# Performance work log

Hardware: AMD Instinct MI355X
Metric: run time of the kernel (lower is better)

The kernel has to match this reference:

```python
import jax, jax.numpy as jnp
import numpy as np

B, S, D = 2048, 8, 1280
K = 1                 # n_components_remove
HIGH_T = 0.6          # PC1_HIGH_ACTIVITY_THRESHOLD
STORM_T = 0.8         # solar_storm_threshold


def setup_inputs() -> dict:
    key = jax.random.key(0)
    k1, k2 = jax.random.split(key, 2)
    features = jax.random.normal(k1, (B, S, D), dtype=jnp.float32)
    kp_index = jax.random.uniform(k2, (B,), dtype=jnp.float32) * 9.0
    cmr_gate = jnp.ones((1,), dtype=jnp.float32)  # nn.Parameter(torch.ones(1))
    return {"features": features, "kp_index": kp_index, "cmr_gate": cmr_gate}


def reference(features, kp_index, cmr_gate):
    # Per-sample standardization over the feature axis (numpy std, ddof=0)
    mu = features.mean(axis=2, keepdims=True)            # (B, S, 1)
    sigma = features.std(axis=2, keepdims=True) + 1e-8   # (B, S, 1)
    fn = (features - mu) / sigma                         # (B, S, D)

    # Batched thin SVD of the (S, D) normalized feature matrix
    U, sv, Vt = jnp.linalg.svd(fn, full_matrices=False)  # (B,S,S), (B,S), (B,S,D)
    var = sv * sv
    pc1_ratio = var[:, 0] / (var.sum(axis=-1) + 1e-8)    # (B,)

    # solar_flag: 0 normal, 1 high activity, 2 storm
    solar_flag = (pc1_ratio >= HIGH_T).astype(jnp.int32) + (pc1_ratio >= STORM_T).astype(jnp.int32)

    # Rank-K reconstruction of the common-mode (solar) component
    low = jnp.einsum('bsk,bk,bkd->bsd', U[:, :, :K], sv[:, :K], Vt[:, :K, :])
    clean = (fn - low) * sigma + mu                      # de-normalized cleaned features

    # Kp-gating: amplify CMR when Kp >= 5
    kp_gate = 1.0 + 0.5 * (kp_index >= 5.0).astype(features.dtype)[:, None, None]
    clean = features + kp_gate * (clean - features)

    # Learnable gate
    gate = jax.nn.sigmoid(cmr_gate)[0]
    features_clean = features + gate * (clean - features)
    return features_clean, pc1_ratio, solar_flag
```

## Files before the change

kernel.cpp:

```cpp
#include <hip/hip_runtime.h>
#include <math.h>


#define SV 8
#define DV 1280
#define D4 320
#define BSTRIDE (SV*DV)
#define GSZ 136
#define SPLIT 4
#define CITER (40/SPLIT)

typedef __attribute__((ext_vector_type(8))) short bf16x8;
typedef __attribute__((ext_vector_type(4))) float f32x4;

union BF8 { bf16x8 v; short s[8]; unsigned u[4]; };

__global__ __launch_bounds__(256, 2)
void cmr_fused(const float* __restrict__ feat,
               const float* __restrict__ kp,
               const float* __restrict__ cmr_gate,
               float* __restrict__ out, int Bn)
{
    __shared__ float lg[SPLIT][2][GSZ];
    __shared__ float lc[2][17];

    const int tid  = threadIdx.x;
    const int lane = tid & 63;
    const int h    = tid >> 6;
    const int pair = blockIdx.x;

    {
        const int m    = lane & 15;
        const int quad = lane >> 4;
        const int bt   = m >> 3;
        const int row  = m & 7;

        const float* __restrict__ fb =
            feat + ((size_t)(pair * 2 + bt)) * BSTRIDE + (size_t)row * DV;

        BF8 ones;
#pragma unroll
        for (int j = 0; j < 4; ++j) ones.u[j] = 0x3F803F80u;

        f32x4 accHH = {0.f, 0.f, 0.f, 0.f};
        f32x4 accHL = {0.f, 0.f, 0.f, 0.f};
        f32x4 accS  = {0.f, 0.f, 0.f, 0.f};

#pragma unroll
        for (int c = 0; c < CITER; ++c) {
            const int k0 = (h * CITER + c) * 32 + quad * 8;
            const float4 x0 = *(const float4*)(fb + k0);
            const float4 x1 = *(const float4*)(fb + k0 + 4);
            float x[8] = {x0.x, x0.y, x0.z, x0.w, x1.x, x1.y, x1.z, x1.w};
            BF8 hi, lo;
#pragma unroll
            for (int j = 0; j < 4; ++j) {
                unsigned hp, lp;
                asm("v_cvt_pk_bf16_f32 %0, %1, %2"
                    : "=v"(hp) : "v"(x[2*j]), "v"(x[2*j+1]));
                const float h0 = __uint_as_float(hp << 16);
                const float h1 = __uint_as_float(hp & 0xFFFF0000u);
                const float l0 = x[2*j]     - h0;
                const float l1 = x[2*j + 1] - h1;
                asm("v_cvt_pk_bf16_f32 %0, %1, %2"
                    : "=v"(lp) : "v"(l0), "v"(l1));
                hi.u[j] = hp;
                lo.u[j] = lp;
            }
            accHH = __builtin_amdgcn_mfma_f32_16x16x32_bf16(hi.v, hi.v,   accHH, 0, 0, 0);
            accHL = __builtin_amdgcn_mfma_f32_16x16x32_bf16(hi.v, lo.v,   accHL, 0, 0, 0);
            accS  = __builtin_amdgcn_mfma_f32_16x16x32_bf16(hi.v, ones.v, accS,  0, 0, 0);
            accS  = __builtin_amdgcn_mfma_f32_16x16x32_bf16(lo.v, ones.v, accS,  0, 0, 0);
        }

        const int colb = (lane & 15) >> 3;
        const int col  = lane & 7;
#pragma unroll
        for (int r = 0; r < 4; ++r) {
            const int rowg = quad * 4 + r;
            if ((rowg >> 3) == colb) {
                lg[h][colb][(rowg & 7) * 8 + col]      = accHH[r];
                lg[h][colb][64 + (rowg & 7) * 8 + col] = accHL[r];
            }
        }
        if ((lane & 15) == 0) {
#pragma unroll
            for (int r = 0; r < 4; ++r) {
                const int rowg = quad * 4 + r;
                lg[h][rowg >> 3][128 + (rowg & 7)] = accS[r];
            }
        }
    }
    __syncthreads();

    if (h == 0 && lane < 2) {
        const int b2 = lane;
        const int b  = pair * 2 + b2;

        float G[8][8], S[8], mu[8], sig[8], rsig[8];
#pragma unroll
        for (int i = 0; i < 8; ++i) {
#pragma unroll
            for (int j = 0; j < 8; ++j) G[i][j] = 0.f;
            S[i] = 0.f;
        }
#pragma unroll
        for (int hh = 0; hh < SPLIT; ++hh) {
            const float* __restrict__ gh = &lg[hh][b2][0];
#pragma unroll
            for (int i = 0; i < 8; ++i) {
#pragma unroll
                for (int j = 0; j < 8; ++j)
                    G[i][j] += gh[i * 8 + j] + gh[64 + i * 8 + j] + gh[64 + j * 8 + i];
                S[i] += gh[128 + i];
            }
        }
        const float invD = 1.f / (float)DV;
#pragma unroll
        for (int i = 0; i < 8; ++i) {
            mu[i] = S[i] * invD;
            const float var = fmaxf(G[i][i] * invD - mu[i] * mu[i], 0.f);
            sig[i]  = sqrtf(var) + 1e-8f;
            rsig[i] = 1.f / sig[i];
        }
#pragma unroll
        for (int i = 0; i < 8; ++i)
#pragma unroll
            for (int j = 0; j < 8; ++j)
                G[i][j] = (G[i][j] - (float)DV * mu[i] * mu[j]) * rsig[i] * rsig[j];

        float tr = 0.f;
#pragma unroll
        for (int i = 0; i < 8; ++i) tr += G[i][i];

        float A[8][8];
        {
            const float rt = 1.f / fmaxf(tr, 1e-30f);
#pragma unroll
            for (int i = 0; i < 8; ++i)
#pragma unroll
                for (int j = 0; j < 8; ++j) A[i][j] = G[i][j] * rt;
        }
#pragma unroll
        for (int t = 0; t < 12; ++t) {
            float Bm[8][8];
            float trB = 0.f;
#pragma unroll
            for (int i = 0; i < 8; ++i)
#pragma unroll
                for (int j = i; j < 8; ++j) {
                    float acc = 0.f;
#pragma unroll
                    for (int k = 0; k < 8; ++k)
                        acc = fmaf(A[i][k], A[j][k], acc);
                    Bm[i][j] = acc;
                    if (i == j) trB += acc;
                }
            const float rt = 1.f / fmaxf(trB, 1e-30f);
#pragma unroll
            for (int i = 0; i < 8; ++i)
#pragma unroll
                for (int j = i; j < 8; ++j) {
                    const float v = Bm[i][j] * rt;
                    A[i][j] = v; A[j][i] = v;
                }
        }
        int bj = 0; float best = A[0][0];
#pragma unroll
        for (int k = 1; k < 8; ++k)
            if (A[k][k] > best) { best = A[k][k]; bj = k; }
        float u[8];
#pragma unroll
        for (int i = 0; i < 8; ++i) {
            float v = A[i][0];
#pragma unroll
            for (int k = 1; k < 8; ++k) v = (bj == k) ? A[i][k] : v;
            u[i] = v;
        }
        {
            float nn = 0.f;
#pragma unroll
            for (int i = 0; i < 8; ++i) nn = fmaf(u[i], u[i], nn);
            const float r = rsqrtf(fmaxf(nn, 1e-30f));
#pragma unroll
            for (int i = 0; i < 8; ++i) u[i] *= r;
        }
#pragma unroll
        for (int it = 0; it < 2; ++it) {
            float y[8]; float ny = 0.f;
#pragma unroll
            for (int i = 0; i < 8; ++i) {
                float acc = 0.f;
#pragma unroll
                for (int k = 0; k < 8; ++k) acc = fmaf(G[i][k], u[k], acc);
                y[i] = acc; ny = fmaf(acc, acc, ny);
            }
            const float r = rsqrtf(fmaxf(ny, 1e-30f));
#pragma unroll
            for (int i = 0; i < 8; ++i) u[i] = y[i] * r;
        }
        float lam = 0.f;
#pragma unroll
        for (int i = 0; i < 8; ++i) {
            float acc = 0.f;
#pragma unroll
            for (int k = 0; k < 8; ++k) acc = fmaf(G[i][k], u[k], acc);
            lam = fmaf(u[i], acc, lam);
        }
        const float pc1 = lam / (tr + 1e-8f);

        const float gate = 1.f / (1.f + expf(-cmr_gate[0]));
        const float kpg  = (kp[b] >= 5.0f) ? 1.5f : 1.0f;
        const float Gt   = gate * kpg;

        float bc = 0.f;
#pragma unroll
        for (int i = 0; i < 8; ++i) bc = fmaf(u[i] * rsig[i], mu[i], bc);

#pragma unroll
        for (int i = 0; i < 8; ++i) {
            lc[b2][i]     = u[i] * rsig[i];
            lc[b2][8 + i] = Gt * sig[i] * u[i];
        }
        lc[b2][16] = bc;
        out[(size_t)Bn * BSTRIDE + b] = pc1;
        out[(size_t)Bn * BSTRIDE + Bn + b] =
            (pc1 >= 0.6f ? 1.f : 0.f) + (pc1 >= 0.8f ? 1.f : 0.f);
    }
    __syncthreads();

    for (int u = tid; u < 2 * D4; u += 256) {
        const int b2  = (u >= D4) ? 1 : 0;
        const int col = u - b2 * D4;

        float a[8], c[8];
#pragma unroll
        for (int s = 0; s < 8; ++s) { a[s] = lc[b2][s]; c[s] = lc[b2][8 + s]; }
        const float bc = lc[b2][16];

        const float4* __restrict__ f4 =
            (const float4*)(feat + (size_t)(pair * 2 + b2) * BSTRIDE);
        float4* __restrict__ o4 =
            (float4*)(out + (size_t)(pair * 2 + b2) * BSTRIDE);

        float4 f[8];
#pragma unroll
        for (int s = 0; s < 8; ++s) f[s] = f4[s * D4 + col];

        float4 p = make_float4(-bc, -bc, -bc, -bc);
#pragma unroll
        for (int s = 0; s < 8; ++s) {
            p.x = fmaf(a[s], f[s].x, p.x);
            p.y = fmaf(a[s], f[s].y, p.y);
            p.z = fmaf(a[s], f[s].z, p.z);
            p.w = fmaf(a[s], f[s].w, p.w);
        }
#pragma unroll
        for (int s = 0; s < 8; ++s) {
            float4 o;
            o.x = fmaf(-c[s], p.x, f[s].x);
            o.y = fmaf(-c[s], p.y, f[s].y);
            o.z = fmaf(-c[s], p.z, f[s].z);
            o.w = fmaf(-c[s], p.w, f[s].w);
            o4[s * D4 + col] = o;
        }
    }
}

extern "C" void kernel_launch(void* const* d_in, const int* in_sizes, int n_in,
                              void* d_out, int out_size, void* d_ws, size_t ws_size,
                              hipStream_t stream) {
    const float* feat = (const float*)d_in[0];
    const float* kp   = (const float*)d_in[1];
    const float* gate = (const float*)d_in[2];
    float* out = (float*)d_out;
    const int Bn = in_sizes[0] / BSTRIDE;
    (void)d_ws; (void)ws_size;

    cmr_fused<<<Bn / 2, 256, 0, stream>>>(feat, kp, gate, out, Bn);
}
```

Baseline: 178.0 us.

## Rewrite as one-wavefront-per-sample kernel holding features in registers

Replaces the 256-thread, two-sample block with a single 64-lane wavefront per batch sample. The wavefront loads the whole 8x1280 slice into registers once, computes the Gram matrix in fp32 FMAs with shuffle reductions in place of split-bf16 MFMAs, and every lane runs the redundant 8x8 eigen solve. The output pass then reuses the register-resident data instead of reloading features from global memory, and LDS and block barriers are gone. In exchange it needs about 160 VGPRs for the data plus the symmetric matrices, which caps occupancy. The serial eigen-solve latency is also no longer hidden behind other waves in the block.

Measured after the change: 171.6 us. 3.6% less time.

```diff
diff --git a/kernel.cpp b/kernel.cpp
--- a/kernel.cpp
+++ b/kernel.cpp
@@ -6,263 +6,201 @@
 #define DV 1280
 #define D4 320
 #define BSTRIDE (SV*DV)
-#define GSZ 136
-#define SPLIT 4
-#define CITER (40/SPLIT)
-
-typedef __attribute__((ext_vector_type(8))) short bf16x8;
-typedef __attribute__((ext_vector_type(4))) float f32x4;
-
-union BF8 { bf16x8 v; short s[8]; unsigned u[4]; };
-
-__global__ __launch_bounds__(256, 2)
-void cmr_fused(const float* __restrict__ feat,
-               const float* __restrict__ kp,
-               const float* __restrict__ cmr_gate,
-               float* __restrict__ out, int Bn)
+
+__device__ __forceinline__ float wsum(float v) {
+    v += __shfl_xor(v, 32);
+    v += __shfl_xor(v, 16);
+    v += __shfl_xor(v, 8);
+    v += __shfl_xor(v, 4);
+    v += __shfl_xor(v, 2);
+    v += __shfl_xor(v, 1);
+    return v;
+}
+
+#define GU(i,k) ((i) <= (k) ? G[i][k] : G[k][i])
+#define AU(i,k) ((i) <= (k) ? A[i][k] : A[k][i])
+
+__global__ __launch_bounds__(64, 1)
+void cmr_wave(const float* __restrict__ feat,
+              const float* __restrict__ kp,
+              const float* __restrict__ cmr_gate,
+              float* __restrict__ out, int Bn)
 {
-    __shared__ float lg[SPLIT][2][GSZ];
-    __shared__ float lc[2][17];
-
-    const int tid  = threadIdx.x;
-    const int lane = tid & 63;
-    const int h    = tid >> 6;
-    const int pair = blockIdx.x;
-
+    const int lane = threadIdx.x;
+    const int b    = blockIdx.x;
+
+    const float4* __restrict__ f4 =
+        (const float4*)(feat + (size_t)b * BSTRIDE);
+
+    float4 f[8][5];
+#pragma unroll
+    for (int s = 0; s < 8; ++s)
+#pragma unroll
+        for (int c = 0; c < 5; ++c)
+            f[s][c] = f4[s * D4 + c * 64 + lane];
+
+    float G[8][8];
+    float S[8];
+#pragma unroll
+    for (int i = 0; i < 8; ++i) {
+        S[i] = 0.f;
+#pragma unroll
+        for (int j = i; j < 8; ++j) G[i][j] = 0.f;
+    }
+#pragma unroll
+    for (int c = 0; c < 5; ++c) {
+#pragma unroll
+        for (int i = 0; i < 8; ++i) {
+            const float4 a = f[i][c];
+            S[i] += (a.x + a.y) + (a.z + a.w);
+#pragma unroll
+            for (int j = i; j < 8; ++j) {
+                const float4 q = f[j][c];
+                G[i][j] = fmaf(a.x, q.x,
+                          fmaf(a.y, q.y,
+                          fmaf(a.z, q.z,
+                          fmaf(a.w, q.w, G[i][j]))));
+            }
+        }
+    }
+#pragma unroll
+    for (int i = 0; i < 8; ++i) {
+        S[i] = wsum(S[i]);
+#pragma unroll
+        for (int j = i; j < 8; ++j) G[i][j] = wsum(G[i][j]);
+    }
+
+    float mu[8], sig[8], rsig[8];
+    const float invD = 1.f / (float)DV;
+#pragma unroll
+    for (int i = 0; i < 8; ++i) {
+        mu[i] = S[i] * invD;
+        const float var = fmaxf(G[i][i] * invD - mu[i] * mu[i], 0.f);
+        sig[i]  = sqrtf(var) + 1e-8f;
+        rsig[i] = 1.f / sig[i];
+    }
+#pragma unroll
+    for (int i = 0; i < 8; ++i)
+#pragma unroll
+        for (int j = i; j < 8; ++j)
+            G[i][j] = (G[i][j] - (float)DV * mu[i] * mu[j]) * rsig[i] * rsig[j];
+
+    float tr = 0.f;
+#pragma unroll
+    for (int i = 0; i < 8; ++i) tr += G[i][i];
+
+    float A[8][8];
     {
-        const int m    = lane & 15;
-        const int quad = lane >> 4;
-        const int bt   = m >> 3;
-        const int row  = m & 7;
-
-        const float* __restrict__ fb =
-            feat + ((size_t)(pair * 2 + bt)) * BSTRIDE + (size_t)row * DV;
-
-        BF8 ones;
-#pragma unroll
-        for (int j = 0; j < 4; ++j) ones.u[j] = 0x3F803F80u;
-
-        f32x4 accHH = {0.f, 0.f, 0.f, 0.f};
-        f32x4 accHL = {0.f, 0.f, 0.f, 0.f};
-        f32x4 accS  = {0.f, 0.f, 0.f, 0.f};
-
-#pragma unroll
-        for (int c = 0; c < CITER; ++c) {
-            const int k0 = (h * CITER + c) * 32 + quad * 8;
-            const float4 x0 = *(const float4*)(fb + k0);
-            const float4 x1 = *(const float4*)(fb + k0 + 4);
-            float x[8] = {x0.x, x0.y, x0.z, x0.w, x1.x, x1.y, x1.z, x1.w};
-            BF8 hi, lo;
-#pragma unroll
-            for (int j = 0; j < 4; ++j) {
-                unsigned hp, lp;
-                asm("v_cvt_pk_bf16_f32 %0, %1, %2"
-                    : "=v"(hp) : "v"(x[2*j]), "v"(x[2*j+1]));
-                const float h0 = __uint_as_float(hp << 16);
-                const float h1 = __uint_as_float(hp & 0xFFFF0000u);
-                const float l0 = x[2*j]     - h0;
-                const float l1 = x[2*j + 1] - h1;
-                asm("v_cvt_pk_bf16_f32 %0, %1, %2"
-                    : "=v"(lp) : "v"(l0), "v"(l1));
-                hi.u[j] = hp;
-                lo.u[j] = lp;
+        const float rt = 1.f / fmaxf(tr, 1e-30f);
+#pragma unroll
+        for (int i = 0; i < 8; ++i)
+#pragma unroll
+            for (int j = i; j < 8; ++j) A[i][j] = G[i][j] * rt;
+    }
+#pragma unroll
+    for (int t = 0; t < 12; ++t) {
+        float Bm[8][8];
+        float trB = 0.f;
+#pragma unroll
+        for (int i = 0; i < 8; ++i)
+#pragma unroll
+            for (int j = i; j < 8; ++j) {
+                float acc = 0.f;
+#pragma unroll
+                for (int k = 0; k < 8; ++k)
+                    acc = fmaf(AU(i, k), AU(j, k), acc);
+                Bm[i][j] = acc;
+                if (i == j) trB += acc;
             }
-            accHH = __builtin_amdgcn_mfma_f32_16x16x32_bf16(hi.v, hi.v,   accHH, 0, 0, 0);
-            accHL = __builtin_amdgcn_mfma_f32_16x16x32_bf16(hi.v, lo.v,   accHL, 0, 0, 0);
-            accS  = __builtin_amdgcn_mfma_f32_16x16x32_bf16(hi.v, ones.v, accS,  0, 0, 0);
-            accS  = __builtin_amdgcn_mfma_f32_16x16x32_bf16(lo.v, ones.v, accS,  0, 0, 0);
-        }
-
-        const int colb = (lane & 15) >> 3;
-        const int col  = lane & 7;
-#pragma unroll
-        for (int r = 0; r < 4; ++r) {
-            const int rowg = quad * 4 + r;
-            if ((rowg >> 3) == colb) {
-                lg[h][colb][(rowg & 7) * 8 + col]      = accHH[r];
-                lg[h][colb][64 + (rowg & 7) * 8 + col] = accHL[r];
-            }
-        }
-        if ((lane & 15) == 0) {
-#pragma unroll
-            for (int r = 0; r < 4; ++r) {
-                const int rowg = quad * 4 + r;
-                lg[h][rowg >> 3][128 + (rowg & 7)] = accS[r];
-            }
-        }
-    }
-    __syncthreads();
-
-    if (h == 0 && lane < 2) {
-        const int b2 = lane;
-        const int b  = pair * 2 + b2;
-
-        float G[8][8], S[8], mu[8], sig[8], rsig[8];
-#pragma unroll
-        for (int i = 0; i < 8; ++i) {
-#pragma unroll
-            for (int j = 0; j < 8; ++j) G[i][j] = 0.f;
-            S[i] = 0.f;
-        }
-#pragma unroll
-        for (int hh = 0; hh < SPLIT; ++hh) {
-            const float* __restrict__ gh = &lg[hh][b2][0];
-#pragma unroll
-            for (int i = 0; i < 8; ++i) {
-#pragma unroll
-                for (int j = 0; j < 8; ++j)
-                    G[i][j] += gh[i * 8 + j] + gh[64 + i * 8 + j] + gh[64 + j * 8 + i];
-                S[i] += gh[128 + i];
-            }
-        }
-        const float invD = 1.f / (float)DV;
-#pragma unroll
-        for (int i = 0; i < 8; ++i) {
-            mu[i] = S[i] * invD;
-            const float var = fmaxf(G[i][i] * invD - mu[i] * mu[i], 0.f);
-            sig[i]  = sqrtf(var) + 1e-8f;
-            rsig[i] = 1.f / sig[i];
-        }
+        const float rt = 1.f / fmaxf(trB, 1e-30f);
 #pragma unroll
         for (int i = 0; i < 8; ++i)
 #pragma unroll
-            for (int j = 0; j < 8; ++j)
-                G[i][j] = (G[i][j] - (float)DV * mu[i] * mu[j]) * rsig[i] * rsig[j];
-
-        float tr = 0.f;
-#pragma unroll
-        for (int i = 0; i < 8; ++i) tr += G[i][i];
-
-        float A[8][8];
-        {
-            const float rt = 1.f / fmaxf(tr, 1e-30f);
-#pragma unroll
-            for (int i = 0; i < 8; ++i)
-#pragma unroll
-                for (int j = 0; j < 8; ++j) A[i][j] = G[i][j] * rt;
-        }
-#pragma unroll
-        for (int t = 0; t < 12; ++t) {
-            float Bm[8][8];
-            float trB = 0.f;
-#pragma unroll
-            for (int i = 0; i < 8; ++i)
-#pragma unroll
-                for (int j = i; j < 8; ++j) {
-                    float acc = 0.f;
-#pragma unroll
-                    for (int k = 0; k < 8; ++k)
-                        acc = fmaf(A[i][k], A[j][k], acc);
-                    Bm[i][j] = acc;
-                    if (i == j) trB += acc;
-                }
-            const float rt = 1.f / fmaxf(trB, 1e-30f);
-#pragma unroll
-            for (int i = 0; i < 8; ++i)
-#pragma unroll
-                for (int j = i; j < 8; ++j) {
-                    const float v = Bm[i][j] * rt;
-                    A[i][j] = v; A[j][i] = v;
-                }
-        }
-        int bj = 0; float best = A[0][0];
-#pragma unroll
-        for (int k = 1; k < 8; ++k)
-            if (A[k][k] > best) { best = A[k][k]; bj = k; }
-        float u[8];
-#pragma unroll
-        for (int i = 0; i < 8; ++i) {
-            float v = A[i][0];
-#pragma unroll
-            for (int k = 1; k < 8; ++k) v = (bj == k) ? A[i][k] : v;
-            u[i] = v;
-        }
-        {
-            float nn = 0.f;
-#pragma unroll
-            for (int i = 0; i < 8; ++i) nn = fmaf(u[i], u[i], nn);
-            const float r = rsqrtf(fmaxf(nn, 1e-30f));
-#pragma unroll
-            for (int i = 0; i < 8; ++i) u[i] *= r;
-        }
-#pragma unroll
-        for (int it = 0; it < 2; ++it) {
-            float y[8]; float ny = 0.f;
-#pragma unroll
-            for (int i = 0; i < 8; ++i) {
-                float acc = 0.f;
-#pragma unroll
-                for (int k = 0; k < 8; ++k) acc = fmaf(G[i][k], u[k], acc);
-                y[i] = acc; ny = fmaf(acc, acc, ny);
-            }
-            const float r = rsqrtf(fmaxf(ny, 1e-30f));
-#pragma unroll
-            for (int i = 0; i < 8; ++i) u[i] = y[i] * r;
-        }
-        float lam = 0.f;
+            for (int j = i; j < 8; ++j) A[i][j] = Bm[i][j] * rt;
+    }
+    int bj = 0; float best = A[0][0];
+#pragma unroll
+    for (int k = 1; k < 8; ++k)
+        if (A[k][k] > best) { best = A[k][k]; bj = k; }
+    float u[8];
+#pragma unroll
+    for (int i = 0; i < 8; ++i) {
+        float v = AU(i, 0);
+#pragma unroll
+        for (int k = 1; k < 8; ++k) v = (bj == k) ? AU(i, k) : v;
+        u[i] = v;
+    }
+    {
+        float nn = 0.f;
+#pragma unroll
+        for (int i = 0; i < 8; ++i) nn = fmaf(u[i], u[i], nn);
+        const float r = rsqrtf(fmaxf(nn, 1e-30f));
+#pragma unroll
+        for (int i = 0; i < 8; ++i) u[i] *= r;
+    }
+#pragma unroll
+    for (int it = 0; it < 2; ++it) {
+        float y[8]; float ny = 0.f;
 #pragma unroll
         for (int i = 0; i < 8; ++i) {
             float acc = 0.f;
 #pragma unroll
-            for (int k = 0; k < 8; ++k) acc = fmaf(G[i][k], u[k], acc);
-            lam = fmaf(u[i], acc, lam);
-        }
-        const float pc1 = lam / (tr + 1e-8f);
-
-        const float gate = 1.f / (1.f + expf(-cmr_gate[0]));
-        const float kpg  = (kp[b] >= 5.0f) ? 1.5f : 1.0f;
-        const float Gt   = gate * kpg;
-
-        float bc = 0.f;
-#pragma unroll
-        for (int i = 0; i < 8; ++i) bc = fmaf(u[i] * rsig[i], mu[i], bc);
-
-#pragma unroll
-        for (int i = 0; i < 8; ++i) {
-            lc[b2][i]     = u[i] * rsig[i];
-            lc[b2][8 + i] = Gt * sig[i] * u[i];
-        }
-        lc[b2][16] = bc;
+            for (int k = 0; k < 8; ++k) acc = fmaf(GU(i, k), u[k], acc);
+            y[i] = acc; ny = fmaf(acc, acc, ny);
+        }
+        const float r = rsqrtf(fmaxf(ny, 1e-30f));
+#pragma unroll
+        for (int i = 0; i < 8; ++i) u[i] = y[i] * r;
+    }
+    float lam = 0.f;
+#pragma unroll
+    for (int i = 0; i < 8; ++i) {
+        float acc = 0.f;
+#pragma unroll
+        for (int k = 0; k < 8; ++k) acc = fmaf(GU(i, k), u[k], acc);
+        lam = fmaf(u[i], acc, lam);
+    }
+    const float pc1 = lam / (tr + 1e-8f);
+
+    const float gate = 1.f / (1.f + expf(-cmr_gate[0]));
+    const float kpg  = (kp[b] >= 5.0f) ? 1.5f : 1.0f;
+    const float Gt   = gate * kpg;
+
+    float av[8], cv[8];
+#pragma unroll
+    for (int i = 0; i < 8; ++i) {
+        av[i] = u[i] * rsig[i];
+        cv[i] = Gt * sig[i] * u[i];
+    }
+    float bc = 0.f;
+#pragma unroll
+    for (int i = 0; i < 8; ++i) bc = fmaf(av[i], mu[i], bc);
+
+    if (lane == 0) {
         out[(size_t)Bn * BSTRIDE + b] = pc1;
         out[(size_t)Bn * BSTRIDE + Bn + b] =
             (pc1 >= 0.6f ? 1.f : 0.f) + (pc1 >= 0.8f ? 1.f : 0.f);
     }
-    __syncthreads();
-
-    for (int u = tid; u < 2 * D4; u += 256) {
-        const int b2  = (u >= D4) ? 1 : 0;
-        const int col = u - b2 * D4;
-
-        float a[8], c[8];
-#pragma unroll
-        for (int s = 0; s < 8; ++s) { a[s] = lc[b2][s]; c[s] = lc[b2][8 + s]; }
-        const float bc = lc[b2][16];
-
-        const float4* __restrict__ f4 =
-            (const float4*)(feat + (size_t)(pair * 2 + b2) * BSTRIDE);
-        float4* __restrict__ o4 =
-            (float4*)(out + (size_t)(pair * 2 + b2) * BSTRIDE);
-
-        float4 f[8];
-#pragma unroll
-        for (int s = 0; s < 8; ++s) f[s] = f4[s * D4 + col];
-
+
+    float4* __restrict__ o4 = (float4*)(out + (size_t)b * BSTRIDE);
+#pragma unroll
+    for (int c = 0; c < 5; ++c) {
         float4 p = make_float4(-bc, -bc, -bc, -bc);
 #pragma unroll
         for (int s = 0; s < 8; ++s) {
-            p.x = fmaf(a[s], f[s].x, p.x);
-            p.y = fmaf(a[s], f[s].y, p.y);
-            p.z = fmaf(a[s], f[s].z, p.z);
-            p.w = fmaf(a[s], f[s].w, p.w);
+            p.x = fmaf(av[s], f[s][c].x, p.x);
+            p.y = fmaf(av[s], f[s][c].y, p.y);
+            p.z = fmaf(av[s], f[s][c].z, p.z);
+            p.w = fmaf(av[s], f[s][c].w, p.w);
         }
 #pragma unroll
         for (int s = 0; s < 8; ++s) {
             float4 o;
-            o.x = fmaf(-c[s], p.x, f[s].x);
-            o.y = fmaf(-c[s], p.y, f[s].y);
-            o.z = fmaf(-c[s], p.z, f[s].z);
-            o.w = fmaf(-c[s], p.w, f[s].w);
-            o4[s * D4 + col] = o;
+            o.x = fmaf(-cv[s], p.x, f[s][c].x);
+            o.y = fmaf(-cv[s], p.y, f[s][c].y);
+            o.z = fmaf(-cv[s], p.z, f[s][c].z);
+            o.w = fmaf(-cv[s], p.w, f[s][c].w);
+            o4[s * D4 + c * 64 + lane] = o;
         }
     }
 }
@@ -277,5 +215,5 @@
     const int Bn = in_sizes[0] / BSTRIDE;
     (void)d_ws; (void)ws_size;
 
-    cmr_fused<<<Bn / 2, 256, 0, stream>>>(feat, kp, gate, out, Bn);
+    cmr_wave<<<Bn, 64, 0, stream>>>(feat, kp, gate, out, Bn);
 }
```
